# Optimization experiments

Measured on AMD Instinct MI355X. Metric: run time of the kernel, lower is better.

Reference implementation:

```python
import jax, jax.numpy as jnp
import numpy as np

# --- configuration (mirrors VFNet cfg) ---
B, NC = 1, 6                     # batch, surround cameras
C_IN, H_F, W_F = 64, 44, 80      # fused feature level (height//8, width//8)
XD, YD, ZD = 100, 100, 20        # voxel dims (x forward, inverse-depth spaced)
X0, X1 = 2.0, 51.5
Y0, Y1 = -25.0, 24.5
Z0, Z1 = -3.0, 2.7
DB, D_STR, D_END = 50, 2.0, 50.0 # projection depth bins (inverse-depth spaced)
VDIM, FOUT = 64, 256             # voxel_pre_dim, feat_out_dim
P = H_F * W_F
EPS = 1e-8


def _axes():
    ego_x = 1.0 / jnp.linspace(1.0 / X1, 1.0 / X0, XD)[::-1]  # ascending, nonuniform
    ego_y = jnp.linspace(Y0, Y1, YD)
    ego_z = jnp.linspace(Z0, Z1, ZD)
    return ego_x, ego_y, ego_z


def _voxel_pts():
    ex, ey, ez = _axes()
    gz, gy, gx = jnp.meshgrid(ez, ey, ex, indexing='ij')      # [Z,Y,X]
    pts = jnp.stack([gx, gy, gz], 0).reshape(3, -1)
    return jnp.concatenate([pts, jnp.ones((1, pts.shape[1]), pts.dtype)], 0)  # [4,N]


def _bilinear2d(img, u, v):
    C, H, W = img.shape
    u0, v0 = jnp.floor(u), jnp.floor(v)
    du, dv = u - u0, v - v0
    u0i = jnp.clip(u0.astype(jnp.int32), 0, W - 1); u1i = jnp.clip(u0i + 1, 0, W - 1)
    v0i = jnp.clip(v0.astype(jnp.int32), 0, H - 1); v1i = jnp.clip(v0i + 1, 0, H - 1)
    g = lambda vi, ui: img[:, vi, ui]
    return (g(v0i, u0i) * (1 - du) * (1 - dv) + g(v0i, u1i) * du * (1 - dv)
            + g(v1i, u0i) * (1 - du) * dv + g(v1i, u1i) * du * dv)


def _nonuniform_index(axis, q):
    # searchsorted + in-bin lerp: metric coord -> continuous index on nonuniform axis
    qc = jnp.clip(q, axis[0], axis[-1] - 1e-6)
    k = jnp.clip(jnp.searchsorted(axis, qc, side='left') - 1, 0, axis.shape[0] - 2)
    t = (qc - axis[k]) / (axis[k + 1] - axis[k] + 1e-12)
    return k.astype(qc.dtype) + t


def _trilinear(vol, xi, yi, zi):
    Cc, Zz, Yy, Xx = vol.shape
    def sp(i, n):
        i0 = jnp.floor(i); t = i - i0
        a = jnp.clip(i0.astype(jnp.int32), 0, n - 1)
        return a, jnp.clip(a + 1, 0, n - 1), t
    x0, x1, tx = sp(xi, Xx); y0, y1, ty = sp(yi, Yy); z0, z1, tz = sp(zi, Zz)
    g = lambda z, y, x: vol[:, z, y, x]
    c0 = (g(z0, y0, x0) * (1 - tx) + g(z0, y0, x1) * tx) * (1 - ty) + (g(z0, y1, x0) * (1 - tx) + g(z0, y1, x1) * tx) * ty
    c1 = (g(z1, y0, x0) * (1 - tx) + g(z1, y0, x1) * tx) * (1 - ty) + (g(z1, y1, x0) * (1 - tx) + g(z1, y1, x1) * tx) * ty
    return c0 * (1 - tz) + c1 * tz


def _conv2d(x, w, b):
    y = jax.lax.conv_general_dilated(x, w, (1, 1), 'SAME', dimension_numbers=('NCHW', 'OIHW', 'NCHW'))
    return y + b[None, :, None, None]


def _conv3d(x, w, b):
    y = jax.lax.conv_general_dilated(x, w, (1, 1, 1), 'SAME', dimension_numbers=('NCDHW', 'OIDHW', 'NCDHW'))
    return y + b[None, :, None, None, None]


def _forward(feats, masks, K, ext, w_ov, b_ov, w_no, b_no, w_fu, b_fu, w_r1, b_r1, w_r2, b_r2):
    ex, ey, ez = _axes()
    vpts = _voxel_pts()                                        # [4,N]
    fm = jnp.concatenate([feats[0], masks[0]], axis=1)         # [NC, C+1, H, W]
    ext_inv = jnp.linalg.inv(ext)

    # --- backproject surround-view features into the nonuniform voxel grid ---
    def per_cam(img, Kc, Ei):
        pix = Kc @ (Ei @ vpts)
        z = pix[2]
        u = pix[0] / (z + EPS); v = pix[1] / (z + EPS)
        valid = (z > EPS) & (u >= 0) & (u <= W_F - 1) & (v >= 0) & (v <= H_F - 1)
        return _bilinear2d(img, u, v) * valid, valid.astype(img.dtype)

    s, valid = jax.vmap(per_cam)(fm, K, ext_inv)               # [NC,C+1,N], [NC,N]
    count = valid.sum(0)
    cat = jnp.concatenate([s[:3].sum(0), s[3:].sum(0)], axis=0)  # [2*(C+1),N]
    ov = jax.nn.elu(w_ov @ cat + b_ov[:, None]) * (count == 2)
    no = jax.nn.elu(w_no @ s.sum(0) + b_no[:, None]) * (count == 1)
    vf = (ov + no).reshape(VDIM, ZD, YD, XD)                   # [64,Z,Y,X]

    # --- nonuniform-x -> uniform-x remap (searchsorted + lerp) + conv3d fusion ---
    xi_axis = _nonuniform_index(ex, jnp.linspace(X0, X1, XD))
    ZI, YI, XI = jnp.meshgrid(jnp.arange(ZD, dtype=vf.dtype), jnp.arange(YD, dtype=vf.dtype), xi_axis, indexing='ij')
    vf_remap = _trilinear(vf, XI, YI, ZI)
    vol = jax.nn.elu(_conv3d(jnp.concatenate([vf, vf_remap], 0)[None], w_fu, b_fu))[0]  # [64,Z,Y,X]

    # --- project fused voxel features into each camera frustum over inv-depth bins ---
    uu, vv = jnp.meshgrid(jnp.arange(W_F), jnp.arange(H_F), indexing='xy')
    pix_grid = jnp.stack([uu.reshape(-1).astype(feats.dtype), vv.reshape(-1).astype(feats.dtype), jnp.ones((P,), feats.dtype)], 0)  # [3,P]
    dbins = 1.0 / jnp.linspace(1.0 / D_END, 1.0 / D_STR, DB)[::-1]  # ascending, inv-depth spaced
    K3inv = jnp.linalg.inv(K[:, :3, :3])

    def per_cam_proj(Ki, Ec):
        dirs = Ki @ pix_grid                                   # [3,P]
        pc = dirs[:, None, :] * dbins[None, :, None]           # [3,D,P]
        pc = jnp.concatenate([pc, jnp.ones((1, DB, P), pc.dtype)], 0)
        pw = (Ec @ pc.reshape(4, -1)).reshape(4, DB, P)        # ego-frame points
        wx, wy, wz = pw[0], pw[1], pw[2]
        xi = _nonuniform_index(ex, wx)
        yi = (wy - Y0) / (Y1 - Y0) * (YD - 1)
        zi = (wz - Z0) / (Z1 - Z0) * (ZD - 1)
        inb = (wx >= X0) & (wx <= X1) & (yi >= 0) & (yi <= YD - 1) & (zi >= 0) & (zi <= ZD - 1)
        samp = _trilinear(vol, xi, yi, zi) * inb               # [64,D,P]
        return samp.reshape(VDIM * DB, H_F, W_F)

    proj = jax.vmap(per_cam_proj)(K3inv, ext)                  # [NC, 64*D, H, W]
    h = jax.nn.elu(_conv2d(proj, w_r1, b_r1))
    return jax.nn.elu(_conv2d(h, w_r2, b_r2))                  # [NC, 256, H, W]


def setup_inputs() -> dict:
    key = jax.random.key(0)
    ks = jax.random.split(key, 8)
    feats = jax.random.normal(ks[0], (B, NC, C_IN, H_F, W_F), jnp.float32)
    masks = jnp.ones((B, NC, 1, H_F, W_F), jnp.float32)
    Kn = np.eye(4, dtype=np.float32)
    Kn[0, 0] = Kn[1, 1] = 40.0; Kn[0, 2] = 40.0; Kn[1, 2] = 22.0  # ~90deg hfov at 80px
    K = np.tile(Kn, (NC, 1, 1))
    ext = np.zeros((NC, 4, 4), dtype=np.float32)
    for i in range(NC):
        th = 2 * np.pi * i / NC
        c, s0 = np.cos(th), np.sin(th)
        R = np.array([[s0, 0, c], [-c, 0, s0], [0, -1, 0]], dtype=np.float32)  # cam(right,down,fwd)->ego
        ext[i, :3, :3] = R
        ext[i, :3, 3] = np.array([c, s0, 0.8], dtype=np.float32)
        ext[i, 3, 3] = 1.0
    w_ov = jax.random.normal(ks[1], (VDIM, 2 * (C_IN + 1)), jnp.float32) / np.sqrt(2 * (C_IN + 1)).astype(np.float32)
    w_no = jax.random.normal(ks[2], (VDIM, C_IN + 1), jnp.float32) / np.sqrt(C_IN + 1).astype(np.float32)
    w_fu = jax.random.normal(ks[3], (VDIM, 2 * VDIM, 3, 3, 3), jnp.float32) / np.sqrt(2 * VDIM * 27).astype(np.float32)
    w_r1 = jax.random.normal(ks[4], (FOUT, VDIM * DB, 3, 3), jnp.float32) / np.sqrt(VDIM * DB * 9).astype(np.float32)
    w_r2 = jax.random.normal(ks[5], (FOUT, FOUT, 3, 3), jnp.float32) / np.sqrt(FOUT * 9).astype(np.float32)
    z = lambda n: jnp.zeros((n,), jnp.float32)
    return {"feats": feats, "masks": masks, "K": jnp.asarray(K), "ext": jnp.asarray(ext),
            "w_ov": w_ov, "b_ov": z(VDIM), "w_no": w_no, "b_no": z(VDIM),
            "w_fu": w_fu, "b_fu": z(VDIM), "w_r1": w_r1, "b_r1": z(FOUT),
            "w_r2": w_r2, "b_r2": z(FOUT)}


def reference(feats, masks, K, ext, w_ov, b_ov, w_no, b_no, w_fu, b_fu, w_r1, b_r1, w_r2, b_r2):
    return _forward(feats, masks, K, ext, w_ov, b_ov, w_no, b_no, w_fu, b_fu, w_r1, b_r1, w_r2, b_r2)
```

## Files before the change

### kernel.cpp

```cpp
#include <hip/hip_runtime.h>
#include <math.h>

#define NCAM 6
#define CIN  64
#define HF   44
#define WF   80
#define PP   (HF*WF)
#define XD   100
#define YD   100
#define ZD   20
#define NVOX (XD*YD*ZD)
#define DBN  50
#define VDIM 64
#define FOUT 256
#define EPSF 1e-8f

typedef _Float16 f16x4 __attribute__((ext_vector_type(4)));
typedef _Float16 f16x8 __attribute__((ext_vector_type(8)));
typedef float    f32x4 __attribute__((ext_vector_type(4)));

#define OFF_KE    0
#define OFF_K3I   96
#define OFF_XI    160
#define OFF_DBIN  260
#define OFF_WOVT  320
#define OFF_WNOT  8640
#define B_VOL     51200UL
#define B_WT1     51200UL
#define B_H       14796800UL
#define B_VIN     25651200UL
#define B_PROJ    25651200UL
#define B_WT2     25651200UL
#define B_WT3     76851200UL
#define B_S       77294592UL
#define B_W2      141294592UL
#define SK        160

__device__ __forceinline__ float eluf(float x) { return x > 0.f ? x : expm1f(x); }

#define AX_A    (1.0f/51.5f)
#define AX_STEP ((0.5f - 1.0f/51.5f)/99.0f)

__device__ __forceinline__ void inv3x3(const float m[9], float o[9]) {
    float a00 = m[4]*m[8] - m[5]*m[7];
    float a10 = m[5]*m[6] - m[3]*m[8];
    float a20 = m[3]*m[7] - m[4]*m[6];
    float det = m[0]*a00 + m[1]*a10 + m[2]*a20;
    float id = 1.0f/det;
    o[0] = a00*id;
    o[1] = (m[2]*m[7] - m[1]*m[8])*id;
    o[2] = (m[1]*m[5] - m[2]*m[4])*id;
    o[3] = a10*id;
    o[4] = (m[0]*m[8] - m[2]*m[6])*id;
    o[5] = (m[2]*m[3] - m[0]*m[5])*id;
    o[6] = a20*id;
    o[7] = (m[1]*m[6] - m[0]*m[7])*id;
    o[8] = (m[0]*m[4] - m[1]*m[3])*id;
}

__global__ __launch_bounds__(256) void setup_kernel(const float* K, const float* ext,
                                                    const float* w_ov, const float* w_no,
                                                    float* ws) {
    int t = threadIdx.x;
    if (t < NCAM) {
        const float* E = ext + t*16;
        float R[9] = {E[0],E[1],E[2], E[4],E[5],E[6], E[8],E[9],E[10]};
        float Ri[9];
        inv3x3(R, Ri);
        float tx=E[3], ty=E[7], tz=E[11];
        float bx = -(Ri[0]*tx + Ri[1]*ty + Ri[2]*tz);
        float by = -(Ri[3]*tx + Ri[4]*ty + Ri[5]*tz);
        float bz = -(Ri[6]*tx + Ri[7]*ty + Ri[8]*tz);
        float Ei[16] = {Ri[0],Ri[1],Ri[2],bx, Ri[3],Ri[4],Ri[5],by, Ri[6],Ri[7],Ri[8],bz, 0,0,0,1};
        const float* Km = K + t*16;
        float* KE = ws + OFF_KE + t*16;
        for (int r=0;r<4;r++)
            for (int c=0;c<4;c++) {
                float s=0.f;
                for (int k=0;k<4;k++) s += Km[r*4+k]*Ei[k*4+c];
                KE[r*4+c]=s;
            }
        float Kr[9] = {Km[0],Km[1],Km[2], Km[4],Km[5],Km[6], Km[8],Km[9],Km[10]};
        float Ki[9];
        inv3x3(Kr, Ki);
        float* KI = ws + OFF_K3I + t*9;
        for (int i=0;i<9;i++) KI[i]=Ki[i];
    }
    if (t >= 64 && t < 64+XD) {
        int x = t-64;
        float ex0 = 1.0f/(AX_A + 99.0f*AX_STEP);
        float exN = 1.0f/AX_A;
        float q = 2.0f + (float)x * (49.5f/99.0f);
        float qc = fminf(fmaxf(q, ex0), exN - 1e-6f);
        float f = 99.0f - (1.0f/qc - AX_A)/AX_STEP;
        int k = min(max((int)floorf(f),0),98);
        float exk  = 1.0f/(AX_A + (float)(99-k)*AX_STEP);
        float exk1 = 1.0f/(AX_A + (float)(98-k)*AX_STEP);
        ws[OFF_XI + x] = (float)k + (qc - exk)/(exk1 - exk + 1e-12f);
    }
    if (t >= 192 && t < 192+DBN) {
        int d = t-192;
        float sa = 1.0f/50.0f;
        float ss = (0.5f - sa)/49.0f;
        ws[OFF_DBIN + d] = 1.0f/(sa + (float)(49-d)*ss);
    }
}

__global__ __launch_bounds__(256) void tw1_kernel(const float* w, _Float16* o) {
    int idx = blockIdx.x*256 + threadIdx.x;
    int cp  = idx % 3200;
    int oc  = (idx/3200) & 255;
    int tap = idx/(3200*256);
    int d = cp >> 6, v = cp & 63;
    o[idx] = (_Float16)w[((size_t)oc*3200 + v*50 + d)*9 + tap];
}
__global__ __launch_bounds__(256) void tw2_kernel(const float* w, _Float16* o) {
    int idx = blockIdx.x*256 + threadIdx.x;
    int ic  = idx & 255;
    int oc  = (idx >> 8) & 255;
    int tap = idx >> 16;
    o[idx] = (_Float16)w[((size_t)oc*256 + ic)*9 + tap];
}
__global__ __launch_bounds__(256) void tw3_kernel(const float* w, _Float16* o) {
    int idx = blockIdx.x*256 + threadIdx.x;
    int ci  = idx & 127;
    int oc  = (idx >> 7) & 63;
    int tap = idx >> 13;
    o[idx] = (_Float16)w[((size_t)oc*128 + ci)*27 + tap];
}
__global__ __launch_bounds__(256) void tw4_kernel(const float* w_ov, const float* w_no,
                                                  _Float16* o) {
    int idx = blockIdx.x*256 + threadIdx.x;
    int k = idx % SK;
    int r = idx / SK;
    float v = 0.f;
    if (r < 64) {
        if (k < 64)                 v = w_ov[r*130 + k];
        else if (k == 64)           v = w_ov[r*130 + 64];
        else if (k >= 66 && k < 130) v = w_ov[r*130 + 65 + (k-66)];
        else if (k == 130)          v = w_ov[r*130 + 129];
    } else {
        int rr = r - 64;
        if (k < 64)                 v = w_no[rr*65 + k];
        else if (k == 64)           v = w_no[rr*65 + 64];
        else if (k >= 66 && k < 130) v = w_no[rr*65 + (k-66)];
        else if (k == 130)          v = w_no[rr*65 + 64];
    }
    o[idx] = (_Float16)v;
}

__global__ __launch_bounds__(256) void gather_kernel(const float* feats, const float* masks,
                                                     const float* ws, _Float16* S) {
    int wave = threadIdx.x >> 6;
    int lane = threadIdx.x & 63;
    int n = blockIdx.x*4 + wave;
    int x = n % XD;
    int y = (n / XD) % YD;
    int z = n / (XD*YD);
    float gx = 1.0f/(AX_A + (float)(99-x)*AX_STEP);
    float gy = -25.0f + (float)y * (49.5f/99.0f);
    float gz = -3.0f  + (float)z * (5.7f/19.0f);

    float sA = 0.f, sB = 0.f, sA64 = 0.f, sB64 = 0.f;
    int cnt = 0;
    for (int cam = 0; cam < NCAM; ++cam) {
        const float* KE = ws + OFF_KE + cam*16;
        float px = KE[0]*gx + KE[1]*gy + KE[2]*gz + KE[3];
        float py = KE[4]*gx + KE[5]*gy + KE[6]*gz + KE[7];
        float pz = KE[8]*gx + KE[9]*gy + KE[10]*gz + KE[11];
        float inv = 1.0f/(pz + EPSF);
        float u = px*inv, v = py*inv;
        bool valid = (pz > EPSF) && (u >= 0.f) && (u <= 79.f) && (v >= 0.f) && (v <= 43.f);
        if (valid) {
            cnt++;
            float u0 = floorf(u), v0 = floorf(v);
            float du = u-u0, dv = v-v0;
            int u0i = min(max((int)u0,0),WF-1), u1i = min(u0i+1,WF-1);
            int v0i = min(max((int)v0,0),HF-1), v1i = min(v0i+1,HF-1);
            float w00=(1.f-du)*(1.f-dv), w01=du*(1.f-dv), w10=(1.f-du)*dv, w11=du*dv;
            int i00=v0i*WF+u0i, i01=v0i*WF+u1i, i10=v1i*WF+u0i, i11=v1i*WF+u1i;
            const float* img = feats + (cam*CIN + lane)*PP;
            float val = w00*img[i00] + w01*img[i01] + w10*img[i10] + w11*img[i11];
            const float* mg = masks + cam*PP;
            float mv = w00*mg[i00] + w01*mg[i01] + w10*mg[i10] + w11*mg[i11];
            if (cam < 3) { sA += val; sA64 += mv; }
            else         { sB += val; sB64 += mv; }
        }
    }
    _Float16* Sp = S + (size_t)n*SK;
    Sp[lane]      = (_Float16)sA;
    Sp[66 + lane] = (_Float16)sB;
    if (lane == 0) { Sp[64] = (_Float16)sA64; Sp[130] = (_Float16)sB64; }
    if (lane == 1) Sp[65] = (_Float16)0.f;
    if (lane >= 3 && lane <= 30) Sp[131 + (lane-3)] = (_Float16)0.f;
    if (lane == 31) Sp[159] = (_Float16)(float)cnt;
}

__global__ __launch_bounds__(256,2) void mlp_kernel(const _Float16* __restrict__ S,
                                                    const _Float16* __restrict__ W2,
                                                    const float* __restrict__ b_ov,
                                                    const float* __restrict__ b_no,
                                                    _Float16* __restrict__ vin) {
    constexpr int WPAD = 168;
    __shared__ __align__(16) _Float16 Wl[128*WPAD];
    int tid = threadIdx.x, lane = tid & 63, wave = tid >> 6;
    int ln = lane & 15, kq = lane >> 4;
    for (int i = tid; i < 128*20; i += 256) {
        int r = i / 20, g8 = i % 20;
        *(f16x8*)(&Wl[r*WPAD + g8*8]) = *(const f16x8*)(W2 + r*SK + g8*8);
    }
    __syncthreads();

    int nbase = blockIdx.x*128 + wave*32;
    f32x4 zero4 = {0.f,0.f,0.f,0.f};
    f32x4 acc[8][2];
    for (int m=0;m<8;m++) for (int t=0;t<2;t++) acc[m][t] = zero4;

    for (int ks = 0; ks < 5; ++ks) {
        int k0 = ks*32 + kq*8;
        f16x8 b0, b1;
        {
            int c0 = min(nbase + ln,      NVOX-1);
            int c1 = min(nbase + 16 + ln, NVOX-1);
            b0 = *(const f16x8*)(S + (size_t)c0*SK + k0);
            b1 = *(const f16x8*)(S + (size_t)c1*SK + k0);
        }
        #pragma unroll
        for (int m = 0; m < 8; ++m) {
            f16x8 a = *(const f16x8*)(&Wl[(m*16 + ln)*WPAD + k0]);
            acc[m][0] = __builtin_amdgcn_mfma_f32_16x16x32_f16(a, b0, acc[m][0], 0,0,0);
            acc[m][1] = __builtin_amdgcn_mfma_f32_16x16x32_f16(a, b1, acc[m][1], 0,0,0);
        }
    }
    #pragma unroll
    for (int t = 0; t < 2; ++t) {
        int col = nbase + t*16 + ln;
        if (col >= NVOX) continue;
        float cnt = (float)S[(size_t)col*SK + 159];
        #pragma unroll
        for (int m = 0; m < 4; ++m) {
            int oc0 = m*16 + kq*4;
            f32x4 bov = *(const f32x4*)(b_ov + oc0);
            f32x4 bno = *(const f32x4*)(b_no + oc0);
            f16x4 s;
            #pragma unroll
            for (int r = 0; r < 4; ++r) {
                float v = 0.f;
                if (cnt == 2.f)      v = eluf(acc[m][t][r]   + bov[r]);
                else if (cnt == 1.f) v = eluf(acc[m+4][t][r] + bno[r]);
                s[r] = (_Float16)v;
            }
            *(f16x4*)(vin + (size_t)col*128 + oc0) = s;
        }
    }
}

__global__ __launch_bounds__(256) void remap_kernel(const float* ws, _Float16* vin) {
    int wave = threadIdx.x >> 6, lane = threadIdx.x & 63;
    int n = blockIdx.x*4 + wave;
    int x = n % XD;
    float xi = ws[OFF_XI + x];
    float fx = floorf(xi);
    float t = xi - fx;
    int x0 = min(max((int)fx,0),XD-1);
    int x1 = min(x0+1, XD-1);
    size_t rowb = (size_t)(n - x)*128;
    float r = (float)vin[rowb + (size_t)x0*128 + lane]*(1.f-t)
            + (float)vin[rowb + (size_t)x1*128 + lane]*t;
    vin[(size_t)n*128 + 64 + lane] = (_Float16)r;
}

__global__ __launch_bounds__(256,2) void conv3d_mfma_kernel(const _Float16* __restrict__ vin,
                                                            const _Float16* __restrict__ wT,
                                                            const float* __restrict__ bias,
                                                            _Float16* __restrict__ vol) {
    __shared__ __align__(16) _Float16 Bs[9*104*36];
    int tid = threadIdx.x, lane = tid & 63, wave = tid >> 6;
    int ln = lane & 15, kq = lane >> 4;
    int y = blockIdx.x % 100, z = blockIdx.x / 100;
    int nt0 = wave*2;
    int ntn = (wave == 3) ? 1 : 2;
    f32x4 zero4 = {0.f,0.f,0.f,0.f};
    f32x4 acc[4][2];
    for (int i=0;i<4;i++) for (int t=0;t<2;t++) acc[i][t] = zero4;

    for (int c0 = 0; c0 < 128; c0 += 32) {
        __syncthreads();
        for (int g = tid; g < 9*104*4; g += 256) {
            int ic8 = g & 3;
            int xe  = (g >> 2) % 104;
            int rid = g / (104*4);
            int xx = xe - 1, yy = y + rid%3 - 1, zz = z + rid/3 - 1;
            f16x8 val = {0,0,0,0,0,0,0,0};
            if (xx >= 0 && xx < 100 && yy >= 0 && yy < 100 && zz >= 0 && zz < 20)
                val = *(const f16x8*)(vin + (size_t)((zz*100 + yy)*100 + xx)*128 + c0 + ic8*8);
            *(f16x8*)(&Bs[(rid*104 + xe)*36 + ic8*8]) = val;
        }
        __syncthreads();
        const _Float16* wp0 = wT + c0 + kq*8;
        f16x8 a0n = *(const f16x8*)(wp0 + (ln+ 0)*128);
        f16x8 a1n = *(const f16x8*)(wp0 + (ln+16)*128);
        f16x8 a2n = *(const f16x8*)(wp0 + (ln+32)*128);
        f16x8 a3n = *(const f16x8*)(wp0 + (ln+48)*128);
        for (int tap = 0; tap < 27; ++tap) {
            f16x8 a0 = a0n, a1 = a1n, a2 = a2n, a3 = a3n;
            if (tap < 26) {
                const _Float16* wp = wT + (size_t)(tap+1)*64*128 + c0 + kq*8;
                a0n = *(const f16x8*)(wp + (ln+ 0)*128);
                a1n = *(const f16x8*)(wp + (ln+16)*128);
                a2n = *(const f16x8*)(wp + (ln+32)*128);
                a3n = *(const f16x8*)(wp + (ln+48)*128);
            }
            int dx = tap % 3, rid = tap / 3;
            for (int t = 0; t < ntn; ++t) {
                int xe = min(16*(nt0+t) + ln + dx, 103);
                f16x8 b = *(const f16x8*)(&Bs[(rid*104 + xe)*36 + kq*8]);
                acc[0][t] = __builtin_amdgcn_mfma_f32_16x16x32_f16(a0, b, acc[0][t], 0,0,0);
                acc[1][t] = __builtin_amdgcn_mfma_f32_16x16x32_f16(a1, b, acc[1][t], 0,0,0);
                acc[2][t] = __builtin_amdgcn_mfma_f32_16x16x32_f16(a2, b, acc[2][t], 0,0,0);
                acc[3][t] = __builtin_amdgcn_mfma_f32_16x16x32_f16(a3, b, acc[3][t], 0,0,0);
            }
        }
    }
    for (int i = 0; i < 4; ++i) {
        int oc0 = i*16 + kq*4;
        f32x4 bv = *(const f32x4*)(bias + oc0);
        for (int t = 0; t < ntn; ++t) {
            int x = 16*(nt0+t) + ln;
            if (x < 100) {
                size_t n = (size_t)(z*100 + y)*100 + x;
                f16x4 s;
                s[0] = (_Float16)eluf(acc[i][t][0] + bv[0]);
                s[1] = (_Float16)eluf(acc[i][t][1] + bv[1]);
                s[2] = (_Float16)eluf(acc[i][t][2] + bv[2]);
                s[3] = (_Float16)eluf(acc[i][t][3] + bv[3]);
                *(f16x4*)(vol + n*64 + oc0) = s;
            }
        }
    }
}

__global__ __launch_bounds__(256) void project_kernel(const float* ws, const float* ext,
                                                      const _Float16* vol, _Float16* proj) {
    __shared__ unsigned s_off[256][8];
    __shared__ float    s_w[256][8];
    int tid = threadIdx.x;
    int item = blockIdx.x*256 + tid;
    int d = item % 50;
    int p = (item/50) % 3520;
    int cam = item / (50*3520);
    {
        float uu = (float)(p % WF), vv = (float)(p / WF);
        const float* KI = ws + OFF_K3I + cam*9;
        float dxr = KI[0]*uu + KI[1]*vv + KI[2];
        float dyr = KI[3]*uu + KI[4]*vv + KI[5];
        float dzr = KI[6]*uu + KI[7]*vv + KI[8];
        float dep = ws[OFF_DBIN + d];
        float cx = dxr*dep, cy = dyr*dep, cz = dzr*dep;
        const float* E = ext + cam*16;
        float wx = E[0]*cx + E[1]*cy + E[2]*cz  + E[3];
        float wy = E[4]*cx + E[5]*cy + E[6]*cz  + E[7];
        float wz = E[8]*cx + E[9]*cy + E[10]*cz + E[11];
        float ex0 = 1.0f/(AX_A + 99.0f*AX_STEP);
        float exN = 1.0f/AX_A;
        float qc = fminf(fmaxf(wx, ex0), exN - 1e-6f);
        float f = 99.0f - (1.0f/qc - AX_A)/AX_STEP;
        int k = min(max((int)floorf(f),0),98);
        float exk  = 1.0f/(AX_A + (float)(99-k)*AX_STEP);
        float exk1 = 1.0f/(AX_A + (float)(98-k)*AX_STEP);
        float xi = (float)k + (qc - exk)/(exk1 - exk + 1e-12f);
        float yi = (wy + 25.0f) * (99.0f/49.5f);
        float zi = (wz + 3.0f)  * (19.0f/5.7f);
        float scale = ((wx >= 2.0f) && (wx <= 51.5f) && (yi >= 0.f) && (yi <= 99.f)
                       && (zi >= 0.f) && (zi <= 19.f)) ? 1.f : 0.f;
        float fx = floorf(xi), fy = floorf(yi), fz = floorf(zi);
        float tx = xi-fx, ty = yi-fy, tz = zi-fz;
        int x0 = min(max((int)fx,0),XD-1), x1 = min(x0+1,XD-1);
        int y0 = min(max((int)fy,0),YD-1), y1 = min(y0+1,YD-1);
        int z0 = min(max((int)fz,0),ZD-1), z1 = min(z0+1,ZD-1);
        s_off[tid][0] = (unsigned)(((z0*YD+y0)*XD+x0)*64); s_w[tid][0] = (1.f-tx)*(1.f-ty)*(1.f-tz)*scale;
        s_off[tid][1] = (unsigned)(((z0*YD+y0)*XD+x1)*64); s_w[tid][1] = tx*(1.f-ty)*(1.f-tz)*scale;
        s_off[tid][2] = (unsigned)(((z0*YD+y1)*XD+x0)*64); s_w[tid][2] = (1.f-tx)*ty*(1.f-tz)*scale;
        s_off[tid][3] = (unsigned)(((z0*YD+y1)*XD+x1)*64); s_w[tid][3] = tx*ty*(1.f-tz)*scale;
        s_off[tid][4] = (unsigned)(((z1*YD+y0)*XD+x0)*64); s_w[tid][4] = (1.f-tx)*(1.f-ty)*tz*scale;
        s_off[tid][5] = (unsigned)(((z1*YD+y0)*XD+x1)*64); s_w[tid][5] = tx*(1.f-ty)*tz*scale;
        s_off[tid][6] = (unsigned)(((z1*YD+y1)*XD+x0)*64); s_w[tid][6] = (1.f-tx)*ty*tz*scale;
        s_off[tid][7] = (unsigned)(((z1*YD+y1)*XD+x1)*64); s_w[tid][7] = tx*ty*tz*scale;
    }
    __syncthreads();
    int wave = tid >> 6, lane = tid & 63;
    size_t outbase = (size_t)blockIdx.x*256 + wave*64;
    for (int j = 0; j < 64; ++j) {
        int it = wave*64 + j;
        float a = 0.f;
        #pragma unroll
        for (int c = 0; c < 8; ++c)
            a += s_w[it][c] * (float)vol[s_off[it][c] + lane];
        proj[(outbase + j)*64 + lane] = (_Float16)a;
    }
}

template<int ICN, bool OUT16>
__global__ __launch_bounds__(256,2) void conv2d_mfma_kernel(const _Float16* __restrict__ in,
                                                            const _Float16* __restrict__ wT,
                                                            const float* __restrict__ bias,
                                                            void* __restrict__ outp) {
    constexpr int NCH = ICN/32;
    constexpr int NSLOT = 6;
    __shared__ __align__(16) _Float16 Bs[2][4*82*36];
    int tid = threadIdx.x, lane = tid & 63, wave = tid >> 6;
    int wm = wave >> 1, wn = wave & 1;
    int ln = lane & 15, kq = lane >> 4;
    int bid = blockIdx.x;
    int ocq = bid & 3;
    int rest = bid >> 2;
    int cam = rest % 6;
    int h0 = (rest / 6)*2;
    int ocb = ocq*64 + wm*32;
    size_t campix0 = (size_t)cam*3520;
    f32x4 zero4 = {0.f,0.f,0.f,0.f};
    f32x4 acc[2][5];
    for (int i=0;i<2;i++) for (int t=0;t<5;t++) acc[i][t] = zero4;

    size_t soff[NSLOT];
    int    slds[NSLOT];
    bool   sok[NSLOT];
    #pragma unroll
    for (int i = 0; i < NSLOT; ++i) {
        int g = tid + i*256;
        if (g < 4*82*4) {
            int ic8 = g & 3;
            int we  = (g >> 2) % 82;
            int re  = g / (82*4);
            int h = h0 - 1 + re;
            int w = we - 1;
            sok[i]  = (h >= 0 && h < HF && w >= 0 && w < WF);
            soff[i] = (campix0 + h*80 + w)*(size_t)ICN + ic8*8;
            slds[i] = (re*82 + we)*36 + ic8*8;
        } else { sok[i] = false; soff[i] = 0; slds[i] = -1; }
    }

    f16x8 sreg[NSLOT];
    #pragma unroll
    for (int i = 0; i < NSLOT; ++i) {
        f16x8 v = {0,0,0,0,0,0,0,0};
        if (sok[i]) v = *(const f16x8*)(in + soff[i]);
        sreg[i] = v;
    }

    const _Float16* wbase0 = wT + (size_t)ocb*ICN + kq*8;
    for (int c = 0; c < NCH; ++c) {
        int buf = c & 1;
        #pragma unroll
        for (int i = 0; i < NSLOT; ++i)
            if (slds[i] >= 0) *(f16x8*)(&Bs[buf][slds[i]]) = sreg[i];
        __syncthreads();
        if (c + 1 < NCH) {
            int c1 = (c+1)*32;
            #pragma unroll
            for (int i = 0; i < NSLOT; ++i) {
                f16x8 v = {0,0,0,0,0,0,0,0};
                if (sok[i]) v = *(const f16x8*)(in + soff[i] + c1);
                sreg[i] = v;
            }
        }
        f16x8 A0[9], A1[9];
        const _Float16* wb = wbase0 + c*32;
        #pragma unroll
        for (int tap = 0; tap < 9; ++tap) {
            const _Float16* wp = wb + (size_t)tap*256*ICN;
            A0[tap] = *(const f16x8*)(wp + (size_t)(ln+ 0)*ICN);
            A1[tap] = *(const f16x8*)(wp + (size_t)(ln+16)*ICN);
        }
        #pragma unroll
        for (int tap = 0; tap < 9; ++tap) {
            int ky = tap/3, kx = tap%3;
            int rbase = (wn + ky)*82 + ln + kx;
            #pragma unroll
            for (int t = 0; t < 5; ++t) {
                f16x8 b = *(const f16x8*)(&Bs[buf][(rbase + 16*t)*36 + kq*8]);
                acc[0][t] = __builtin_amdgcn_mfma_f32_16x16x32_f16(A0[tap], b, acc[0][t], 0,0,0);
                acc[1][t] = __builtin_amdgcn_mfma_f32_16x16x32_f16(A1[tap], b, acc[1][t], 0,0,0);
            }
        }
    }
    int pixrow = h0 + wn;
    for (int i = 0; i < 2; ++i) {
        int oc0 = ocb + i*16 + kq*4;
        f32x4 bv = *(const f32x4*)(bias + oc0);
        for (int t = 0; t < 5; ++t) {
            int pix = pixrow*80 + 16*t + ln;
            float v0 = eluf(acc[i][t][0] + bv[0]);
            float v1 = eluf(acc[i][t][1] + bv[1]);
            float v2 = eluf(acc[i][t][2] + bv[2]);
            float v3 = eluf(acc[i][t][3] + bv[3]);
            if (OUT16) {
                f16x4 s; s[0]=(_Float16)v0; s[1]=(_Float16)v1; s[2]=(_Float16)v2; s[3]=(_Float16)v3;
                *(f16x4*)((_Float16*)outp + (campix0 + pix)*256 + oc0) = s;
            } else {
                float* op = (float*)outp + ((size_t)(cam*256 + oc0))*PP + pix;
                op[0] = v0; op[PP] = v1; op[2*PP] = v2; op[3*PP] = v3;
            }
        }
    }
}

extern "C" void kernel_launch(void* const* d_in, const int* in_sizes, int n_in,
                              void* d_out, int out_size, void* d_ws, size_t ws_size,
                              hipStream_t stream) {
    const float* feats = (const float*)d_in[0];
    const float* masks = (const float*)d_in[1];
    const float* K     = (const float*)d_in[2];
    const float* ext   = (const float*)d_in[3];
    const float* w_ov  = (const float*)d_in[4];
    const float* b_ov  = (const float*)d_in[5];
    const float* w_no  = (const float*)d_in[6];
    const float* b_no  = (const float*)d_in[7];
    const float* w_fu  = (const float*)d_in[8];
    const float* b_fu  = (const float*)d_in[9];
    const float* w_r1  = (const float*)d_in[10];
    const float* b_r1  = (const float*)d_in[11];
    const float* w_r2  = (const float*)d_in[12];
    const float* b_r2  = (const float*)d_in[13];
    char* base = (char*)d_ws;
    float*    wsf  = (float*)base;
    _Float16* vol  = (_Float16*)(base + B_VOL);
    _Float16* wT1  = (_Float16*)(base + B_WT1);
    _Float16* h    = (_Float16*)(base + B_H);
    _Float16* vin  = (_Float16*)(base + B_VIN);
    _Float16* proj = (_Float16*)(base + B_PROJ);
    _Float16* wT2  = (_Float16*)(base + B_WT2);
    _Float16* wT3  = (_Float16*)(base + B_WT3);
    _Float16* Sbuf = (_Float16*)(base + B_S);
    _Float16* W2   = (_Float16*)(base + B_W2);
    float* out = (float*)d_out;

    setup_kernel<<<1, 256, 0, stream>>>(K, ext, w_ov, w_no, wsf);
    tw3_kernel<<<(27*64*128)/256, 256, 0, stream>>>(w_fu, wT3);
    tw4_kernel<<<(128*SK)/256, 256, 0, stream>>>(w_ov, w_no, W2);
    gather_kernel<<<NVOX/4, 256, 0, stream>>>(feats, masks, wsf, Sbuf);
    mlp_kernel<<<(NVOX + 127)/128, 256, 0, stream>>>(Sbuf, W2, b_ov, b_no, vin);
    remap_kernel<<<NVOX/4, 256, 0, stream>>>(wsf, vin);
    conv3d_mfma_kernel<<<ZD*YD, 256, 0, stream>>>(vin, wT3, b_fu, vol);
    project_kernel<<<(NCAM*PP*DBN)/256, 256, 0, stream>>>(wsf, ext, vol, proj);
    tw1_kernel<<<(9*256*3200)/256, 256, 0, stream>>>(w_r1, wT1);
    conv2d_mfma_kernel<3200, true><<<4*NCAM*22, 256, 0, stream>>>(proj, wT1, b_r1, h);
    tw2_kernel<<<(9*256*256)/256, 256, 0, stream>>>(w_r2, wT2);
    conv2d_mfma_kernel<256, false><<<4*NCAM*22, 256, 0, stream>>>(h, wT2, b_r2, out);
}
```

Measured before the change: 1.674 ms.

## Transpose features to channel-last fp16 for gather and double-buffer conv2d weight loads

Adds a transpose kernel that converts camera features from channel-major fp32 to pixel-major fp16. The gather kernel's per-lane channel reads then become contiguous rather than strided by the plane size, which reduces scattered global loads. The conv2d MFMA kernel now double-buffers its weight fragments in registers, prefetching the next chunk's weights while the current chunk computes. The cost is an extra transpose pass, fp16 rounding of features before interpolation, and higher register pressure in the conv kernel.

After: 2.768 ms. 1.65x slower.

```diff
diff --git a/kernel.cpp b/kernel.cpp
--- a/kernel.cpp
+++ b/kernel.cpp
@@ -23,8 +23,6 @@
 #define OFF_K3I   96
 #define OFF_XI    160
 #define OFF_DBIN  260
-#define OFF_WOVT  320
-#define OFF_WNOT  8640
 #define B_VOL     51200UL
 #define B_WT1     51200UL
 #define B_H       14796800UL
@@ -34,6 +32,7 @@
 #define B_WT3     76851200UL
 #define B_S       77294592UL
 #define B_W2      141294592UL
+#define B_FT      141335552UL
 #define SK        160
 
 __device__ __forceinline__ float eluf(float x) { return x > 0.f ? x : expm1f(x); }
@@ -59,7 +58,6 @@
 }
 
 __global__ __launch_bounds__(256) void setup_kernel(const float* K, const float* ext,
-                                                    const float* w_ov, const float* w_no,
                                                     float* ws) {
     int t = threadIdx.x;
     if (t < NCAM) {
@@ -148,8 +146,15 @@
     }
     o[idx] = (_Float16)v;
 }
-
-__global__ __launch_bounds__(256) void gather_kernel(const float* feats, const float* masks,
+__global__ __launch_bounds__(256) void tw5_kernel(const float* feats, _Float16* o) {
+    int idx = blockIdx.x*256 + threadIdx.x;
+    int ch = idx & 63;
+    int p  = (idx >> 6) % PP;
+    int cam = idx / (64*PP);
+    o[idx] = (_Float16)feats[((size_t)(cam*64 + ch))*PP + p];
+}
+
+__global__ __launch_bounds__(256) void gather_kernel(const _Float16* featsT, const float* masks,
                                                      const float* ws, _Float16* S) {
     int wave = threadIdx.x >> 6;
     int lane = threadIdx.x & 63;
@@ -179,8 +184,11 @@
             int v0i = min(max((int)v0,0),HF-1), v1i = min(v0i+1,HF-1);
             float w00=(1.f-du)*(1.f-dv), w01=du*(1.f-dv), w10=(1.f-du)*dv, w11=du*dv;
             int i00=v0i*WF+u0i, i01=v0i*WF+u1i, i10=v1i*WF+u0i, i11=v1i*WF+u1i;
-            const float* img = feats + (cam*CIN + lane)*PP;
-            float val = w00*img[i00] + w01*img[i01] + w10*img[i10] + w11*img[i11];
+            const _Float16* img = featsT + (size_t)cam*PP*64;
+            float val = w00*(float)img[(size_t)i00*64 + lane]
+                      + w01*(float)img[(size_t)i01*64 + lane]
+                      + w10*(float)img[(size_t)i10*64 + lane]
+                      + w11*(float)img[(size_t)i11*64 + lane];
             const float* mg = masks + cam*PP;
             float mv = w00*mg[i00] + w01*mg[i01] + w10*mg[i10] + w11*mg[i11];
             if (cam < 3) { sA += val; sA64 += mv; }
@@ -447,10 +455,17 @@
         if (sok[i]) v = *(const f16x8*)(in + soff[i]);
         sreg[i] = v;
     }
-
     const _Float16* wbase0 = wT + (size_t)ocb*ICN + kq*8;
+    f16x8 A0[2][9], A1[2][9];
+    #pragma unroll
+    for (int tap = 0; tap < 9; ++tap) {
+        const _Float16* wp = wbase0 + (size_t)tap*256*ICN;
+        A0[0][tap] = *(const f16x8*)(wp + (size_t)(ln+ 0)*ICN);
+        A1[0][tap] = *(const f16x8*)(wp + (size_t)(ln+16)*ICN);
+    }
+
     for (int c = 0; c < NCH; ++c) {
-        int buf = c & 1;
+        int buf = c & 1, nxt = buf ^ 1;
         #pragma unroll
         for (int i = 0; i < NSLOT; ++i)
             if (slds[i] >= 0) *(f16x8*)(&Bs[buf][slds[i]]) = sreg[i];
@@ -463,14 +478,13 @@
                 if (sok[i]) v = *(const f16x8*)(in + soff[i] + c1);
                 sreg[i] = v;
             }
-        }
-        f16x8 A0[9], A1[9];
-        const _Float16* wb = wbase0 + c*32;
-        #pragma unroll
-        for (int tap = 0; tap < 9; ++tap) {
-            const _Float16* wp = wb + (size_t)tap*256*ICN;
-            A0[tap] = *(const f16x8*)(wp + (size_t)(ln+ 0)*ICN);
-            A1[tap] = *(const f16x8*)(wp + (size_t)(ln+16)*ICN);
+            const _Float16* wb = wbase0 + c1;
+            #pragma unroll
+            for (int tap = 0; tap < 9; ++tap) {
+                const _Float16* wp = wb + (size_t)tap*256*ICN;
+                A0[nxt][tap] = *(const f16x8*)(wp + (size_t)(ln+ 0)*ICN);
+                A1[nxt][tap] = *(const f16x8*)(wp + (size_t)(ln+16)*ICN);
+            }
         }
         #pragma unroll
         for (int tap = 0; tap < 9; ++tap) {
@@ -479,8 +493,8 @@
             #pragma unroll
             for (int t = 0; t < 5; ++t) {
                 f16x8 b = *(const f16x8*)(&Bs[buf][(rbase + 16*t)*36 + kq*8]);
-                acc[0][t] = __builtin_amdgcn_mfma_f32_16x16x32_f16(A0[tap], b, acc[0][t], 0,0,0);
-                acc[1][t] = __builtin_amdgcn_mfma_f32_16x16x32_f16(A1[tap], b, acc[1][t], 0,0,0);
+                acc[0][t] = __builtin_amdgcn_mfma_f32_16x16x32_f16(A0[buf][tap], b, acc[0][t], 0,0,0);
+                acc[1][t] = __builtin_amdgcn_mfma_f32_16x16x32_f16(A1[buf][tap], b, acc[1][t], 0,0,0);
             }
         }
     }
@@ -533,12 +547,14 @@
     _Float16* wT3  = (_Float16*)(base + B_WT3);
     _Float16* Sbuf = (_Float16*)(base + B_S);
     _Float16* W2   = (_Float16*)(base + B_W2);
+    _Float16* fT   = (_Float16*)(base + B_FT);
     float* out = (float*)d_out;
 
-    setup_kernel<<<1, 256, 0, stream>>>(K, ext, w_ov, w_no, wsf);
+    setup_kernel<<<1, 256, 0, stream>>>(K, ext, wsf);
     tw3_kernel<<<(27*64*128)/256, 256, 0, stream>>>(w_fu, wT3);
     tw4_kernel<<<(128*SK)/256, 256, 0, stream>>>(w_ov, w_no, W2);
-    gather_kernel<<<NVOX/4, 256, 0, stream>>>(feats, masks, wsf, Sbuf);
+    tw5_kernel<<<(NCAM*PP*64)/256, 256, 0, stream>>>(feats, fT);
+    gather_kernel<<<NVOX/4, 256, 0, stream>>>(fT, masks, wsf, Sbuf);
     mlp_kernel<<<(NVOX + 127)/128, 256, 0, stream>>>(Sbuf, W2, b_ov, b_no, vin);
     remap_kernel<<<NVOX/4, 256, 0, stream>>>(wsf, vin);
     conv3d_mfma_kernel<<<ZD*YD, 256, 0, stream>>>(vin, wT3, b_fu, vol);
```
